# Kernel tuning notes

Measured on AMD Instinct MI355X. Metric: run time of the kernel, lower is better.

## Reference

```python
import jax, jax.numpy as jnp
import numpy as np

B, N, D, H = 8, 577, 768, 12
HD = D // H
SCALE = HD ** -0.5
LN_EPS = 1e-5


def layer_norm(x, w, b):
    mu = jnp.mean(x, -1, keepdims=True)
    var = jnp.mean((x - mu) ** 2, -1, keepdims=True)
    return (x - mu) * jax.lax.rsqrt(var + LN_EPS) * w + b


def wasserstein_distance_matmul(mean1, cov1, mean2, cov2):
    # all [B,H,N,hd]; returns [B,H,N,N]
    m1_2 = jnp.sum(mean1 ** 2, -1, keepdims=True)
    m2_2 = jnp.sum(mean2 ** 2, -1, keepdims=True)
    ret = -2.0 * jnp.einsum('bhnd,bhmd->bhnm', mean1, mean2) + m1_2 + jnp.swapaxes(m2_2, -1, -2)
    c1s = jnp.sqrt(jnp.clip(cov1, 1e-24))
    c2s = jnp.sqrt(jnp.clip(cov2, 1e-24))
    cov_ret = (-2.0 * jnp.einsum('bhnd,bhmd->bhnm', c1s, c2s)
               + jnp.sum(cov1, -1, keepdims=True)
               + jnp.swapaxes(jnp.sum(cov2, -1, keepdims=True), -1, -2))
    return ret + cov_ret


def setup_inputs() -> dict:
    key = jax.random.key(0)
    ks = jax.random.split(key, 20)
    s = 0.02
    return {
        'x_mean': jax.random.normal(ks[0], (B, N, D), jnp.float32),
        'x_cov': jax.random.normal(ks[1], (B, N, D), jnp.float32),
        'rel_pos_bias': jax.random.normal(ks[2], (1, H, N, N), jnp.float32),
        'norm1_w': jnp.ones((D,), jnp.float32),
        'norm1_b': jnp.zeros((D,), jnp.float32),
        'qkv_w': jax.random.normal(ks[3], (3 * D, D), jnp.float32) * s,
        'proj_w': jax.random.normal(ks[4], (D, D), jnp.float32) * s,
        'proj_b': jnp.zeros((D,), jnp.float32),
        'cov_proj_w': jax.random.normal(ks[5], (D, D), jnp.float32) * s,
        'cov_proj_b': jnp.zeros((D,), jnp.float32),
        'norm2_w': jnp.ones((D,), jnp.float32),
        'norm2_b': jnp.zeros((D,), jnp.float32),
        'fc1_w': jax.random.normal(ks[6], (4 * D, D), jnp.float32) * s,
        'fc1_b': jnp.zeros((4 * D,), jnp.float32),
        'fc2_w': jax.random.normal(ks[7], (D, 4 * D), jnp.float32) * s,
        'fc2_b': jnp.zeros((D,), jnp.float32),
        'gamma1': 0.1 * jnp.ones((D,), jnp.float32),
        'gamma2': 0.1 * jnp.ones((D,), jnp.float32),
    }


def _split_heads(t):
    # [B,N,3D] -> q,k,v each [B,H,N,hd]
    t = t.reshape(B, N, 3, H, HD).transpose(2, 0, 3, 1, 4)
    return t[0], t[1], t[2]


def attention(xm, xc, rel_pos_bias, qkv_w, proj_w, proj_b, cov_proj_w, cov_proj_b):
    qkv = xm @ qkv_w.T                                  # [B,N,3D]
    q, k, v = _split_heads(qkv)
    cov_qkv = jax.nn.elu(xc @ qkv_w.T) + 1.0            # same weights for cov stream
    cov_q, cov_k, cov_v = _split_heads(cov_qkv)
    q = q * SCALE
    attn = -wasserstein_distance_matmul(q, cov_q, k, cov_k)
    attn = jax.nn.sigmoid(attn + 1e-24)
    attn = jax.nn.softmax(attn + rel_pos_bias, axis=-1)  # [B,H,N,N]
    mean_ctx = jnp.einsum('bhnm,bhmd->bhnd', attn, v).transpose(0, 2, 1, 3).reshape(B, N, D)
    cov_ctx = jnp.einsum('bhnm,bhmd->bhnd', attn ** 2, cov_v).transpose(0, 2, 1, 3).reshape(B, N, D)
    mean_out = mean_ctx @ proj_w.T + proj_b
    cov_out = cov_ctx @ cov_proj_w.T + cov_proj_b
    return mean_out, cov_out


def mlp(x, fc1_w, fc1_b, fc2_w, fc2_b):
    h = jax.nn.gelu(x @ fc1_w.T + fc1_b, approximate=False)
    return h @ fc2_w.T + fc2_b


def reference(x_mean, x_cov, rel_pos_bias, norm1_w, norm1_b, qkv_w, proj_w, proj_b,
              cov_proj_w, cov_proj_b, norm2_w, norm2_b, fc1_w, fc1_b, fc2_w, fc2_b,
              gamma1, gamma2):
    mean, cov = attention(layer_norm(x_mean, norm1_w, norm1_b),
                          layer_norm(x_cov, norm1_w, norm1_b),
                          rel_pos_bias, qkv_w, proj_w, proj_b, cov_proj_w, cov_proj_b)
    x_mean = x_mean + gamma1 * mean
    fcm = gamma2 * mlp(layer_norm(x_mean, norm2_w, norm2_b), fc1_w, fc1_b, fc2_w, fc2_b)
    x_cov = x_cov + gamma1 * cov
    fcc = gamma2 * mlp(layer_norm(x_cov, norm2_w, norm2_b), fc1_w, fc1_b, fc2_w, fc2_b)
    return (x_mean + fcm, x_cov + fcc)
```

## Files before the change

### kernel.cpp

```cpp
#include <hip/hip_runtime.h>
#include <hip/hip_bf16.h>
#include <math.h>
#include <stdint.h>

typedef __bf16 bf16;
typedef __attribute__((ext_vector_type(8))) __bf16 bf16x8;
typedef __attribute__((ext_vector_type(4))) float f32x4;

typedef __attribute__((address_space(1))) void gas_void;
typedef __attribute__((address_space(3))) void las_void;

#define DEV __device__ __forceinline__

static constexpr int B_ = 8, N_ = 577, D_ = 768, H_ = 12;
static constexpr int M_ = B_ * N_;
static constexpr int MP_ = 4736;
static constexpr int NP_ = 640;
static constexpr int BH_ = B_ * H_;
static constexpr float SCALE_ = 0.125f;

DEV void async_cp16(const void* g, void* l) {
  __builtin_amdgcn_global_load_lds((gas_void*)g, (las_void*)l, 16, 0, 0);
}
DEV float fast_rcp(float x) { return __builtin_amdgcn_rcpf(x); }
DEV float elu1(float x) { return x > 0.0f ? x + 1.0f : __expf(x); }
DEV float fast_gelu(float x) {
  const float x2 = x * x;
  const float z = x * fmaf(0.0713548826f, x2, 1.5957691216f);
  return x * fast_rcp(1.0f + __expf(-z));
}

__global__ __launch_bounds__(256) void cvt_kernel(const float* __restrict__ src,
                                                  bf16* __restrict__ dst, int n) {
  int i = blockIdx.x * 256 + threadIdx.x;
  if (i < n) dst[i] = (bf16)src[i];
}

__global__ __launch_bounds__(256) void ln_kernel(const float* __restrict__ x,
                                                 const float* __restrict__ w,
                                                 const float* __restrict__ bp,
                                                 bf16* __restrict__ out) {
  const int row = blockIdx.x;
  const int t = threadIdx.x;
  const float* xr = x + (size_t)row * D_;
  float v0 = xr[t], v1 = xr[t + 256], v2 = xr[t + 512];
  float s = v0 + v1 + v2;
  float ss = v0 * v0 + v1 * v1 + v2 * v2;
#pragma unroll
  for (int m = 32; m >= 1; m >>= 1) {
    s += __shfl_down(s, m);
    ss += __shfl_down(ss, m);
  }
  __shared__ float red[8];
  if ((t & 63) == 0) { red[t >> 6] = s; red[4 + (t >> 6)] = ss; }
  __syncthreads();
  s = red[0] + red[1] + red[2] + red[3];
  ss = red[4] + red[5] + red[6] + red[7];
  const float mu = s * (1.0f / D_);
  float var = ss * (1.0f / D_) - mu * mu;
  var = fmaxf(var, 0.0f);
  const float rs = rsqrtf(var + 1e-5f);
  bf16* orow = out + (size_t)row * D_;
  orow[t]       = (bf16)((v0 - mu) * rs * w[t]       + bp[t]);
  orow[t + 256] = (bf16)((v1 - mu) * rs * w[t + 256] + bp[t + 256]);
  orow[t + 512] = (bf16)((v2 - mu) * rs * w[t + 512] + bp[t + 512]);
}

enum { EP_BF16 = 0, EP_PROJ = 1, EP_GELU = 2, EP_FC2 = 3 };

template <int EP>
__global__ __launch_bounds__(256) void gemm_bt(
    const bf16* __restrict__ A, const bf16* __restrict__ W0,
    const bf16* __restrict__ W1, int Nn, int K, int gx,
    const float* __restrict__ bias0, const float* __restrict__ bias1,
    const float* __restrict__ gamma,
    const float* __restrict__ resid0, const float* __restrict__ resid1,
    bf16* __restrict__ Cb, float* __restrict__ Cf0, float* __restrict__ Cf1) {
  __shared__ __align__(16) bf16 As[2][128 * 32];
  __shared__ __align__(16) bf16 Bs[2][128 * 32];
  const int nwg = gridDim.x;
  const int o = blockIdx.x;
  const int q = nwg >> 3, r = nwg & 7, xcd = o & 7;
  const int flat = (xcd < r ? xcd * (q + 1) : r * (q + 1) + (xcd - r) * q) + (o >> 3);
  const int bx = flat % gx, by = flat / gx;

  const int t = threadIdx.x;
  const int lane = t & 63, wv = t >> 6;
  const int ln = lane & 15, kg = lane >> 4;
  const int wr = wv >> 1, wc = wv & 1;
  const int s = (int)(by >= (MP_ / 128));
  const bf16* W = s ? W1 : W0;
  const size_t brow = (size_t)by * 128;
  const size_t bcol = (size_t)bx * 128;
  const int r0 = t >> 2, gsl = t & 3;
  const bf16* A0 = A + (brow + r0) * (size_t)K + gsl * 8;
  const bf16* A1 = A + (brow + r0 + 64) * (size_t)K + gsl * 8;
  const bf16* W0p = W + (bcol + r0) * (size_t)K + gsl * 8;
  const bf16* W1p = W + (bcol + r0 + 64) * (size_t)K + gsl * 8;

  auto stage = [&](int buf, int kk) {
    async_cp16(A0 + kk, &As[buf][(wv * 64) * 8]);
    async_cp16(A1 + kk, &As[buf][(256 + wv * 64) * 8]);
    async_cp16(W0p + kk, &Bs[buf][(wv * 64) * 8]);
    async_cp16(W1p + kk, &Bs[buf][(256 + wv * 64) * 8]);
  };

  f32x4 acc[4][4] = {};
  const int nt = K >> 5;
  stage(0, 0);
  __syncthreads();
  int cur = 0;
  for (int tt = 0; tt < nt; ++tt) {
    if (tt + 1 < nt) stage(cur ^ 1, (tt + 1) * 32);
    bf16x8 af[4], bfr[4];
#pragma unroll
    for (int i = 0; i < 4; i++)
      af[i] = *(const bf16x8*)&As[cur][(wr * 64 + i * 16 + ln) * 32 + kg * 8];
#pragma unroll
    for (int j = 0; j < 4; j++)
      bfr[j] = *(const bf16x8*)&Bs[cur][(wc * 64 + j * 16 + ln) * 32 + kg * 8];
#pragma unroll
    for (int i = 0; i < 4; i++)
#pragma unroll
      for (int j = 0; j < 4; j++)
        acc[i][j] = __builtin_amdgcn_mfma_f32_16x16x32_bf16(af[i], bfr[j], acc[i][j], 0, 0, 0);
    __syncthreads();
    cur ^= 1;
  }

  const float* biasS = s ? bias1 : bias0;
  const float* residS = s ? resid1 : resid0;
  float* CfS = s ? Cf1 : Cf0;
#pragma unroll
  for (int i = 0; i < 4; i++) {
    const int rb = (int)brow + wr * 64 + i * 16 + kg * 4;
#pragma unroll
    for (int j = 0; j < 4; j++) {
      const int col = (int)bcol + wc * 64 + j * 16 + ln;
#pragma unroll
      for (int rr = 0; rr < 4; rr++) {
        const int row = rb + rr;
        float v = acc[i][j][rr];
        if (EP == EP_BF16) {
          Cb[(size_t)row * Nn + col] = (bf16)v;
        } else if (EP == EP_GELU) {
          v += biasS[col];
          Cb[(size_t)row * Nn + col] = (bf16)fast_gelu(v);
        } else {
          const int r2 = row - s * MP_;
          if (r2 < M_) {
            v += biasS[col];
            if (EP == EP_PROJ) {
              CfS[(size_t)r2 * Nn + col] = residS[(size_t)r2 * Nn + col] + gamma[col] * v;
            } else {
              CfS[(size_t)r2 * Nn + col] += gamma[col] * v;
            }
          }
        }
      }
    }
  }
}

__global__ __launch_bounds__(256) void prep_kernel(
    const bf16* __restrict__ qm, const bf16* __restrict__ qc,
    bf16* __restrict__ Qcat, bf16* __restrict__ Kcat,
    bf16* __restrict__ Vt, bf16* __restrict__ CVt,
    float* __restrict__ rowt, float* __restrict__ colt) {
  const int n0 = blockIdx.x * 64;
  const int h = blockIdx.y, b = blockIdx.z;
  const int bh = b * H_ + h;
  const int t = threadIdx.x;
  const int nl = t >> 2, c = t & 3;
  const int n = n0 + nl;
  const bool valid = n < N_;
  __shared__ bf16 vts[64][72], cvts[64][72];
  float q2 = 0.f, cqs = 0.f, k2 = 0.f, cks = 0.f;
  bf16 qo[16], sqo[16], ko[16], sko[16];
  if (valid) {
    const size_t ro = (size_t)(b * N_ + n) * 2304 + h * 64 + c * 16;
#pragma unroll
    for (int half = 0; half < 2; half++) {
      bf16x8 qv8 = *(const bf16x8*)(qm + ro + half * 8);
      bf16x8 kv8 = *(const bf16x8*)(qm + ro + 768 + half * 8);
      bf16x8 vv8 = *(const bf16x8*)(qm + ro + 1536 + half * 8);
      bf16x8 cq8 = *(const bf16x8*)(qc + ro + half * 8);
      bf16x8 ck8 = *(const bf16x8*)(qc + ro + 768 + half * 8);
      bf16x8 cv8 = *(const bf16x8*)(qc + ro + 1536 + half * 8);
#pragma unroll
      for (int i = 0; i < 8; i++) {
        const int d = half * 8 + i;
        float qv = (float)qv8[i] * SCALE_;
        float kv = (float)kv8[i];
        float cq1 = elu1((float)cq8[i]);
        float ck1 = elu1((float)ck8[i]);
        q2 += qv * qv; cqs += cq1; k2 += kv * kv; cks += ck1;
        qo[d] = (bf16)qv; sqo[d] = (bf16)sqrtf(fmaxf(cq1, 1e-24f));
        ko[d] = (bf16)kv; sko[d] = (bf16)sqrtf(fmaxf(ck1, 1e-24f));
        vts[nl][c * 16 + d] = vv8[i];
        cvts[nl][c * 16 + d] = (bf16)elu1((float)cv8[i]);
      }
    }
  } else {
#pragma unroll
    for (int d = 0; d < 16; d++) {
      qo[d] = (bf16)0.f; sqo[d] = (bf16)0.f; ko[d] = (bf16)0.f; sko[d] = (bf16)0.f;
      vts[nl][c * 16 + d] = (bf16)0.f; cvts[nl][c * 16 + d] = (bf16)0.f;
    }
  }
  {
    bf16* qrow = Qcat + ((size_t)bh * NP_ + n) * 128;
    bf16* krow = Kcat + ((size_t)bh * NP_ + n) * 128;
#pragma unroll
    for (int d = 0; d < 16; d++) {
      qrow[c * 16 + d] = qo[d];
      qrow[64 + c * 16 + d] = sqo[d];
      krow[c * 16 + d] = ko[d];
      krow[64 + c * 16 + d] = sko[d];
    }
  }
  float rt = q2 + cqs, ct = k2 + cks;
  rt += __shfl_xor(rt, 1); rt += __shfl_xor(rt, 2);
  ct += __shfl_xor(ct, 1); ct += __shfl_xor(ct, 2);
  if (c == 0) { rowt[(size_t)bh * NP_ + n] = rt; colt[(size_t)bh * NP_ + n] = ct; }
  __syncthreads();
  const int drow = t >> 2;
  const size_t vb = ((size_t)bh * 64 + drow) * NP_ + n0 + c * 16;
#pragma unroll
  for (int i = 0; i < 16; i++) {
    Vt[vb + i] = vts[c * 16 + i][drow];
    CVt[vb + i] = cvts[c * 16 + i][drow];
  }
}

__global__ __launch_bounds__(256) void attn_kernel(
    const bf16* __restrict__ Qcat, const bf16* __restrict__ Kcat,
    const bf16* __restrict__ Vt, const bf16* __restrict__ CVt,
    const float* __restrict__ rowt, const float* __restrict__ colt,
    const bf16* __restrict__ bias,
    bf16* __restrict__ ctxm, bf16* __restrict__ ctxc) {
  const int id = blockIdx.x;
  const int xcd = id & 7, slot = id >> 3;
  const int g = xcd + 8 * (slot / 10);
  const int it = slot % 10;
  const int b = g / H_, h = g % H_;
  const int bh = g;
  const int i0 = it * 64;
  const int t = threadIdx.x;
  const int lane = t & 63, w = t >> 6;
  const int ln = lane & 15, kg = lane >> 4;
  __shared__ __align__(16) bf16 Ks[64 * 128];
  __shared__ __align__(16) bf16 Vs[64 * 64];
  __shared__ __align__(16) bf16 CVs[64 * 64];
  __shared__ __align__(16) bf16 Ps[64 * 72];

  const bf16* Qg = Qcat + (size_t)bh * NP_ * 128;
  const bf16* Kg = Kcat + (size_t)bh * NP_ * 128;
  const bf16* Vg = Vt + (size_t)bh * 64 * NP_;
  const bf16* CVg = CVt + (size_t)bh * 64 * NP_;

#pragma unroll
  for (int qq = 0; qq < 4; qq++) {
    const int idx = qq * 256 + t;
    const int row = idx >> 4, sl = idx & 15;
    async_cp16(Qg + (size_t)(i0 + row) * 128 + ((sl ^ (row & 7)) * 8),
               &Ks[(qq * 256 + w * 64) * 8]);
  }
  __syncthreads();
  bf16x8 aq[4];
  {
    const int row = w * 16 + ln;
#pragma unroll
    for (int kc = 0; kc < 4; kc++) {
      const int slot2 = kc * 4 + kg;
      aq[kc] = *(const bf16x8*)&Ks[row * 128 + ((slot2 ^ (row & 7)) * 8)];
    }
  }
  float rt[4];
#pragma unroll
  for (int r = 0; r < 4; r++) rt[r] = rowt[(size_t)bh * NP_ + i0 + w * 16 + kg * 4 + r];

  f32x4 accm[4] = {}, accc[4] = {};
  float den[4] = {0.f, 0.f, 0.f, 0.f};
  const int igb = i0 + w * 16 + kg * 4;

  for (int jt = 0; jt < 10; jt++) {
    const int j0 = jt * 64;
    __syncthreads();
#pragma unroll
    for (int qq = 0; qq < 4; qq++) {
      const int idx = qq * 256 + t;
      const int row = idx >> 4, sl = idx & 15;
      async_cp16(Kg + (size_t)(j0 + row) * 128 + ((sl ^ (row & 7)) * 8),
                 &Ks[(qq * 256 + w * 64) * 8]);
    }
#pragma unroll
    for (int qq = 0; qq < 2; qq++) {
      const int idx = qq * 256 + t;
      const int row = idx >> 3, sl = idx & 7;
      async_cp16(Vg + (size_t)row * NP_ + j0 + ((sl ^ (row & 7)) * 8),
                 &Vs[(qq * 256 + w * 64) * 8]);
      async_cp16(CVg + (size_t)row * NP_ + j0 + ((sl ^ (row & 7)) * 8),
                 &CVs[(qq * 256 + w * 64) * 8]);
    }
    float bb[4][4], ctb[4];
#pragma unroll
    for (int js = 0; js < 4; js++) {
      const int jg = j0 + js * 16 + ln;
      const int jc = jg < N_ ? jg : N_ - 1;
      ctb[js] = colt[(size_t)bh * NP_ + jg];
#pragma unroll
      for (int r = 0; r < 4; r++) {
        const int ic = (igb + r) < N_ ? (igb + r) : N_ - 1;
        bb[js][r] = (float)bias[((size_t)h * N_ + ic) * N_ + jc];
      }
    }
    __syncthreads();
#pragma unroll
    for (int js = 0; js < 4; js++) {
      f32x4 sv = {};
#pragma unroll
      for (int kc = 0; kc < 4; kc++) {
        const int row = js * 16 + ln;
        const int slot2 = kc * 4 + kg;
        bf16x8 bk = *(const bf16x8*)&Ks[row * 128 + ((slot2 ^ (row & 7)) * 8)];
        sv = __builtin_amdgcn_mfma_f32_16x16x32_bf16(aq[kc], bk, sv, 0, 0, 0);
      }
      const int jg = j0 + js * 16 + ln;
#pragma unroll
      for (int r = 0; r < 4; r++) {
        const float S = 2.0f * sv[r] - rt[r] - ctb[js];
        const float sig = fast_rcp(1.0f + __expf(-S));
        float e = __expf(sig + bb[js][r]);
        if (jg >= N_) e = 0.0f;
        const bf16 eb = (bf16)e;
        den[r] += (float)eb;
        Ps[(w * 16 + kg * 4 + r) * 72 + js * 16 + ln] = eb;
      }
    }
#pragma unroll
    for (int ks = 0; ks < 2; ks++) {
      const int prow = w * 16 + ln;
      bf16x8 pa = *(const bf16x8*)&Ps[prow * 72 + ks * 32 + kg * 8];
      bf16x8 p2a;
#pragma unroll
      for (int i = 0; i < 8; i++) {
        const float pf = (float)pa[i];
        p2a[i] = (bf16)(pf * pf);
      }
#pragma unroll
      for (int nt = 0; nt < 4; nt++) {
        const int vrow = nt * 16 + ln;
        const int slot2 = ks * 4 + kg;
        bf16x8 vb = *(const bf16x8*)&Vs[vrow * 64 + ((slot2 ^ (vrow & 7)) * 8)];
        bf16x8 cvb = *(const bf16x8*)&CVs[vrow * 64 + ((slot2 ^ (vrow & 7)) * 8)];
        accm[nt] = __builtin_amdgcn_mfma_f32_16x16x32_bf16(pa, vb, accm[nt], 0, 0, 0);
        accc[nt] = __builtin_amdgcn_mfma_f32_16x16x32_bf16(p2a, cvb, accc[nt], 0, 0, 0);
      }
    }
  }
#pragma unroll
  for (int r = 0; r < 4; r++) {
    float d = den[r];
    d += __shfl_xor(d, 1); d += __shfl_xor(d, 2);
    d += __shfl_xor(d, 4); d += __shfl_xor(d, 8);
    den[r] = d;
  }
#pragma unroll
  for (int r = 0; r < 4; r++) {
    const int ig = i0 + w * 16 + kg * 4 + r;
    if (ig < N_) {
      const float inv = fast_rcp(den[r]);
      const float inv2 = inv * inv;
      const size_t base = (size_t)(b * N_ + ig) * D_ + h * 64;
#pragma unroll
      for (int nt = 0; nt < 4; nt++) {
        ctxm[base + nt * 16 + ln] = (bf16)(accm[nt][r] * inv);
        ctxc[base + nt * 16 + ln] = (bf16)(accc[nt][r] * inv2);
      }
    }
  }
}

extern "C" void kernel_launch(void* const* d_in, const int* in_sizes, int n_in,
                              void* d_out, int out_size, void* d_ws, size_t ws_size,
                              hipStream_t stream) {
  const float* x_mean = (const float*)d_in[0];
  const float* x_cov  = (const float*)d_in[1];
  const float* rpb    = (const float*)d_in[2];
  const float* n1w    = (const float*)d_in[3];
  const float* n1b    = (const float*)d_in[4];
  const float* qkvw   = (const float*)d_in[5];
  const float* projw  = (const float*)d_in[6];
  const float* projb  = (const float*)d_in[7];
  const float* cprojw = (const float*)d_in[8];
  const float* cprojb = (const float*)d_in[9];
  const float* n2w    = (const float*)d_in[10];
  const float* n2b    = (const float*)d_in[11];
  const float* fc1w   = (const float*)d_in[12];
  const float* fc1b   = (const float*)d_in[13];
  const float* fc2w   = (const float*)d_in[14];
  const float* fc2b   = (const float*)d_in[15];
  const float* g1     = (const float*)d_in[16];
  const float* g2     = (const float*)d_in[17];
  (void)in_sizes; (void)n_in; (void)out_size; (void)ws_size;

  char* ws = (char*)d_ws;
  size_t off = 0;
  auto take = [&](size_t bytes) {
    char* p = ws + off;
    off += (bytes + 255) & ~(size_t)255;
    return p;
  };
  bf16* wq   = (bf16*)take((size_t)2304 * 768 * 2);
  bf16* wp   = (bf16*)take((size_t)768 * 768 * 2);
  bf16* wcp  = (bf16*)take((size_t)768 * 768 * 2);
  bf16* wf1  = (bf16*)take((size_t)3072 * 768 * 2);
  bf16* wf2  = (bf16*)take((size_t)768 * 3072 * 2);
  bf16* xln  = (bf16*)take((size_t)2 * MP_ * 768 * 2);
  char* R    = take((size_t)2 * MP_ * 3072 * 2);
  bf16* qkvb = (bf16*)R;
  bf16* hbuf = (bf16*)R;
  bf16* biasb = (bf16*)(R + (size_t)2 * MP_ * 2304 * 2);
  bf16* Qcat = (bf16*)take((size_t)BH_ * NP_ * 128 * 2);
  bf16* Kcat = (bf16*)take((size_t)BH_ * NP_ * 128 * 2);
  bf16* Vt   = (bf16*)take((size_t)BH_ * 64 * NP_ * 2);
  bf16* CVt  = (bf16*)take((size_t)BH_ * 64 * NP_ * 2);
  float* rowt = (float*)take((size_t)BH_ * NP_ * 4);
  float* colt = (float*)take((size_t)BH_ * NP_ * 4);
  bf16* ctx  = (bf16*)take((size_t)2 * MP_ * 768 * 2);

  float* outm = (float*)d_out;
  float* outc = outm + (size_t)M_ * D_;

  cvt_kernel<<<(2304 * 768 + 255) / 256, 256, 0, stream>>>(qkvw, wq, 2304 * 768);
  cvt_kernel<<<(768 * 768 + 255) / 256, 256, 0, stream>>>(projw, wp, 768 * 768);
  cvt_kernel<<<(768 * 768 + 255) / 256, 256, 0, stream>>>(cprojw, wcp, 768 * 768);
  cvt_kernel<<<(3072 * 768 + 255) / 256, 256, 0, stream>>>(fc1w, wf1, 3072 * 768);
  cvt_kernel<<<(768 * 3072 + 255) / 256, 256, 0, stream>>>(fc2w, wf2, 768 * 3072);
  cvt_kernel<<<(H_ * N_ * N_ + 255) / 256, 256, 0, stream>>>(rpb, biasb, H_ * N_ * N_);
  ln_kernel<<<M_, 256, 0, stream>>>(x_mean, n1w, n1b, xln);
  ln_kernel<<<M_, 256, 0, stream>>>(x_cov, n1w, n1b, xln + (size_t)MP_ * 768);
  gemm_bt<EP_BF16><<<18 * 74, 256, 0, stream>>>(xln, wq, wq, 2304, 768, 18,
      nullptr, nullptr, nullptr, nullptr, nullptr, qkvb, nullptr, nullptr);
  prep_kernel<<<dim3(10, 12, 8), 256, 0, stream>>>(
      qkvb, qkvb + (size_t)MP_ * 2304, Qcat, Kcat, Vt, CVt, rowt, colt);
  attn_kernel<<<960, 256, 0, stream>>>(Qcat, Kcat, Vt, CVt, rowt, colt, biasb,
                                       ctx, ctx + (size_t)MP_ * 768);
  gemm_bt<EP_PROJ><<<6 * 74, 256, 0, stream>>>(ctx, wp, wcp, 768, 768, 6,
      projb, cprojb, g1, x_mean, x_cov, nullptr, outm, outc);
  ln_kernel<<<M_, 256, 0, stream>>>(outm, n2w, n2b, xln);
  ln_kernel<<<M_, 256, 0, stream>>>(outc, n2w, n2b, xln + (size_t)MP_ * 768);
  gemm_bt<EP_GELU><<<24 * 74, 256, 0, stream>>>(xln, wf1, wf1, 3072, 768, 24,
      fc1b, fc1b, nullptr, nullptr, nullptr, hbuf, nullptr, nullptr);
  gemm_bt<EP_FC2><<<6 * 74, 256, 0, stream>>>(hbuf, wf2, wf2, 768, 3072, 6,
      fc2b, fc2b, g2, nullptr, nullptr, nullptr, outm, outc);
}
```

Baseline: 401.0 us.

## Triple-buffer GEMM LDS pipeline with vmcnt waits and vectorize weight conversion

The GEMM main loop goes from double-buffered LDS staging with two __syncthreads per step to a three-stage ring. It prefetches two K-tiles ahead and uses explicit s_waitcnt vmcnt plus a single s_barrier per step, so more global-to-LDS loads are in flight while MFMA runs. K becomes a template parameter so the loop unrolls by three. The cvt kernel also switches to float4 loads with 64-bit stores. LDS use grows from 32KB to 48KB per block, which may lower occupancy, and the hand-written vmcnt counts and barrier placement carry a correctness risk.

```diff
diff --git a/kernel.cpp b/kernel.cpp
--- a/kernel.cpp
+++ b/kernel.cpp
@@ -31,9 +31,13 @@
 }
 
 __global__ __launch_bounds__(256) void cvt_kernel(const float* __restrict__ src,
-                                                  bf16* __restrict__ dst, int n) {
-  int i = blockIdx.x * 256 + threadIdx.x;
-  if (i < n) dst[i] = (bf16)src[i];
+                                                  bf16* __restrict__ dst, int n4) {
+  const int i = blockIdx.x * 256 + threadIdx.x;
+  if (i < n4) {
+    const float4 v = ((const float4*)src)[i];
+    bf16 o[4] = {(bf16)v.x, (bf16)v.y, (bf16)v.z, (bf16)v.w};
+    *(uint64_t*)(dst + (size_t)i * 4) = *(const uint64_t*)o;
+  }
 }
 
 __global__ __launch_bounds__(256) void ln_kernel(const float* __restrict__ x,
@@ -68,16 +72,16 @@
 
 enum { EP_BF16 = 0, EP_PROJ = 1, EP_GELU = 2, EP_FC2 = 3 };
 
-template <int EP>
+template <int EP, int K>
 __global__ __launch_bounds__(256) void gemm_bt(
     const bf16* __restrict__ A, const bf16* __restrict__ W0,
-    const bf16* __restrict__ W1, int Nn, int K, int gx,
+    const bf16* __restrict__ W1, int Nn, int gx,
     const float* __restrict__ bias0, const float* __restrict__ bias1,
     const float* __restrict__ gamma,
     const float* __restrict__ resid0, const float* __restrict__ resid1,
     bf16* __restrict__ Cb, float* __restrict__ Cf0, float* __restrict__ Cf1) {
-  __shared__ __align__(16) bf16 As[2][128 * 32];
-  __shared__ __align__(16) bf16 Bs[2][128 * 32];
+  __shared__ __align__(16) bf16 As[3][128 * 32];
+  __shared__ __align__(16) bf16 Bs[3][128 * 32];
   const int nwg = gridDim.x;
   const int o = blockIdx.x;
   const int q = nwg >> 3, r = nwg & 7, xcd = o & 7;
@@ -106,26 +110,35 @@
   };
 
   f32x4 acc[4][4] = {};
-  const int nt = K >> 5;
+  constexpr int nt = K >> 5;
+  static_assert(nt % 3 == 0, "K/32 must be divisible by 3");
   stage(0, 0);
-  __syncthreads();
-  int cur = 0;
-  for (int tt = 0; tt < nt; ++tt) {
-    if (tt + 1 < nt) stage(cur ^ 1, (tt + 1) * 32);
-    bf16x8 af[4], bfr[4];
-#pragma unroll
-    for (int i = 0; i < 4; i++)
-      af[i] = *(const bf16x8*)&As[cur][(wr * 64 + i * 16 + ln) * 32 + kg * 8];
-#pragma unroll
-    for (int j = 0; j < 4; j++)
-      bfr[j] = *(const bf16x8*)&Bs[cur][(wc * 64 + j * 16 + ln) * 32 + kg * 8];
-#pragma unroll
-    for (int i = 0; i < 4; i++)
+  stage(1, 32);
+#pragma unroll 1
+  for (int tb = 0; tb < nt; tb += 3) {
+#pragma unroll
+    for (int u = 0; u < 3; u++) {
+      const int tt = tb + u;
+      if (tt + 1 < nt) {
+        asm volatile("s_waitcnt vmcnt(4)" ::: "memory");
+      } else {
+        asm volatile("s_waitcnt vmcnt(0)" ::: "memory");
+      }
+      __builtin_amdgcn_s_barrier();
+      bf16x8 af[4], bfr[4];
+#pragma unroll
+      for (int i = 0; i < 4; i++)
+        af[i] = *(const bf16x8*)&As[u][(wr * 64 + i * 16 + ln) * 32 + kg * 8];
 #pragma unroll
       for (int j = 0; j < 4; j++)
-        acc[i][j] = __builtin_amdgcn_mfma_f32_16x16x32_bf16(af[i], bfr[j], acc[i][j], 0, 0, 0);
-    __syncthreads();
-    cur ^= 1;
+        bfr[j] = *(const bf16x8*)&Bs[u][(wc * 64 + j * 16 + ln) * 32 + kg * 8];
+#pragma unroll
+      for (int i = 0; i < 4; i++)
+#pragma unroll
+        for (int j = 0; j < 4; j++)
+          acc[i][j] = __builtin_amdgcn_mfma_f32_16x16x32_bf16(af[i], bfr[j], acc[i][j], 0, 0, 0);
+      if (tt + 2 < nt) stage((u + 2) % 3, (tt + 2) * 32);
+    }
   }
 
   const float* biasS = s ? bias1 : bias0;
@@ -433,26 +446,26 @@
   float* outm = (float*)d_out;
   float* outc = outm + (size_t)M_ * D_;
 
-  cvt_kernel<<<(2304 * 768 + 255) / 256, 256, 0, stream>>>(qkvw, wq, 2304 * 768);
-  cvt_kernel<<<(768 * 768 + 255) / 256, 256, 0, stream>>>(projw, wp, 768 * 768);
-  cvt_kernel<<<(768 * 768 + 255) / 256, 256, 0, stream>>>(cprojw, wcp, 768 * 768);
-  cvt_kernel<<<(3072 * 768 + 255) / 256, 256, 0, stream>>>(fc1w, wf1, 3072 * 768);
-  cvt_kernel<<<(768 * 3072 + 255) / 256, 256, 0, stream>>>(fc2w, wf2, 768 * 3072);
-  cvt_kernel<<<(H_ * N_ * N_ + 255) / 256, 256, 0, stream>>>(rpb, biasb, H_ * N_ * N_);
+  cvt_kernel<<<(2304 * 768 / 4 + 255) / 256, 256, 0, stream>>>(qkvw, wq, 2304 * 768 / 4);
+  cvt_kernel<<<(768 * 768 / 4 + 255) / 256, 256, 0, stream>>>(projw, wp, 768 * 768 / 4);
+  cvt_kernel<<<(768 * 768 / 4 + 255) / 256, 256, 0, stream>>>(cprojw, wcp, 768 * 768 / 4);
+  cvt_kernel<<<(3072 * 768 / 4 + 255) / 256, 256, 0, stream>>>(fc1w, wf1, 3072 * 768 / 4);
+  cvt_kernel<<<(768 * 3072 / 4 + 255) / 256, 256, 0, stream>>>(fc2w, wf2, 768 * 3072 / 4);
+  cvt_kernel<<<(H_ * N_ * N_ / 4 + 255) / 256, 256, 0, stream>>>(rpb, biasb, H_ * N_ * N_ / 4);
   ln_kernel<<<M_, 256, 0, stream>>>(x_mean, n1w, n1b, xln);
   ln_kernel<<<M_, 256, 0, stream>>>(x_cov, n1w, n1b, xln + (size_t)MP_ * 768);
-  gemm_bt<EP_BF16><<<18 * 74, 256, 0, stream>>>(xln, wq, wq, 2304, 768, 18,
+  gemm_bt<EP_BF16, 768><<<18 * 74, 256, 0, stream>>>(xln, wq, wq, 2304, 18,
       nullptr, nullptr, nullptr, nullptr, nullptr, qkvb, nullptr, nullptr);
   prep_kernel<<<dim3(10, 12, 8), 256, 0, stream>>>(
       qkvb, qkvb + (size_t)MP_ * 2304, Qcat, Kcat, Vt, CVt, rowt, colt);
   attn_kernel<<<960, 256, 0, stream>>>(Qcat, Kcat, Vt, CVt, rowt, colt, biasb,
                                        ctx, ctx + (size_t)MP_ * 768);
-  gemm_bt<EP_PROJ><<<6 * 74, 256, 0, stream>>>(ctx, wp, wcp, 768, 768, 6,
+  gemm_bt<EP_PROJ, 768><<<6 * 74, 256, 0, stream>>>(ctx, wp, wcp, 768, 6,
       projb, cprojb, g1, x_mean, x_cov, nullptr, outm, outc);
   ln_kernel<<<M_, 256, 0, stream>>>(outm, n2w, n2b, xln);
   ln_kernel<<<M_, 256, 0, stream>>>(outc, n2w, n2b, xln + (size_t)MP_ * 768);
-  gemm_bt<EP_GELU><<<24 * 74, 256, 0, stream>>>(xln, wf1, wf1, 3072, 768, 24,
+  gemm_bt<EP_GELU, 768><<<24 * 74, 256, 0, stream>>>(xln, wf1, wf1, 3072, 24,
       fc1b, fc1b, nullptr, nullptr, nullptr, hbuf, nullptr, nullptr);
-  gemm_bt<EP_FC2><<<6 * 74, 256, 0, stream>>>(hbuf, wf2, wf2, 768, 3072, 6,
+  gemm_bt<EP_FC2, 3072><<<6 * 74, 256, 0, stream>>>(hbuf, wf2, wf2, 768, 6,
       fc2b, fc2b, g2, nullptr, nullptr, nullptr, outm, outc);
 }
```

Result: faster. 385.7 us (-3.8%).
